# Performance work log

Measured on AMD Instinct MI355X. Metric: run time of the kernel, lower is better.

## Reference

```python
import jax, jax.numpy as jnp
import numpy as np

N_DELTA, N_THETA, N_GAMMA = 64, 128, 512
N_TOTAL = N_DELTA + N_THETA + N_GAMMA  # 704
N_CLASSES = 1000
N_STEPS = 5
DT = 0.01
COUPLING = 2.0      # coupling_strength
PAC_DT = 0.3        # delta->theta phase-amplitude coupling depth
PAC_TG = 0.3        # theta->gamma phase-amplitude coupling depth
SPARSITY = 0.1      # PhaseToRateConverter sparsity (fraction of active units)
SHARP = 10.0        # softness of the 'soft' sparsification gate
TWO_PI = 2.0 * np.pi
B = 65536


def setup_inputs() -> dict:
    key = jax.random.key(0)
    k1, k2, k3, k4 = jax.random.split(key, 4)
    x = jax.random.normal(k1, (B, N_TOTAL), dtype=jnp.float32)
    # per-sample random initial phases in [0,1), scaled to [0,2pi) inside reference
    phase0 = jax.random.uniform(k2, (B, N_TOTAL), dtype=jnp.float32)
    W = jax.random.normal(k3, (N_CLASSES, N_TOTAL), dtype=jnp.float32) * 0.02
    b = jax.random.normal(k4, (N_CLASSES,), dtype=jnp.float32) * 0.02
    return {"x": x, "phase0": phase0, "W": W, "b": b}


def _kuramoto(phi):
    # mean-field within-band Kuramoto coupling: K * mean_j sin(phi_j - phi_i)
    S = jnp.mean(jnp.sin(phi), axis=-1, keepdims=True)
    C = jnp.mean(jnp.cos(phi), axis=-1, keepdims=True)
    return COUPLING * (S * jnp.cos(phi) - C * jnp.sin(phi))


def _mean_phase(phi):
    # circular mean phase of a band, shape (B,1)
    return jnp.arctan2(jnp.mean(jnp.sin(phi), axis=-1, keepdims=True),
                       jnp.mean(jnp.cos(phi), axis=-1, keepdims=True))


def _forward(x, phase0, W, b):
    freqs = jnp.concatenate([
        jnp.linspace(1.0, 4.0, N_DELTA),    # delta band Hz
        jnp.linspace(4.0, 8.0, N_THETA),    # theta band Hz
        jnp.linspace(30.0, 80.0, N_GAMMA),  # gamma band Hz
    ]).astype(x.dtype)
    phi = phase0 * TWO_PI                       # (B, N_TOTAL)
    amp = 1.0 + jnp.abs(x) * 0.01               # amplitude seeded by |x|*0.01 on unit base
    d = slice(0, N_DELTA)
    t = slice(N_DELTA, N_DELTA + N_THETA)
    g = slice(N_DELTA + N_THETA, N_TOTAL)

    def step(carry, _):
        phi, amp = carry
        dphi = TWO_PI * freqs + jnp.concatenate(
            [_kuramoto(phi[:, d]), _kuramoto(phi[:, t]), _kuramoto(phi[:, g])], axis=-1)
        psi_d = _mean_phase(phi[:, d])
        psi_t = _mean_phase(phi[:, t])
        # PAC: theta amplitude driven by delta phase, gamma amplitude by theta phase
        damp = jnp.concatenate([
            jnp.zeros_like(amp[:, d]),
            PAC_DT * amp[:, t] * jnp.cos(psi_d),
            PAC_TG * amp[:, g] * jnp.cos(psi_t),
        ], axis=-1)
        phi_new = jnp.mod(phi + DT * dphi, TWO_PI)
        amp_new = amp + DT * damp
        return (phi_new, amp_new), None

    (phi, amp), _ = jax.lax.scan(step, (phi, amp), None, length=N_STEPS)

    # PhaseToRateConverter, mode='soft': raw rate then soft top-(sparsity) gate
    raw = amp * 0.5 * (1.0 + jnp.cos(phi))                              # (B, N_TOTAL)
    thr = jnp.quantile(raw, 1.0 - SPARSITY, axis=-1, keepdims=True)    # per-sample threshold
    rate = raw * jax.nn.sigmoid((raw - thr) * SHARP)
    return rate @ W.T + b                                               # (B, N_CLASSES)


def reference(x, phase0, W, b):
    return _forward(x, phase0, W, b)
```

## Files before the change

kernel.cpp:

```cpp
#include <hip/hip_runtime.h>

#define NB 65536
#define NTOT 704
#define NCLS 1000
#define NPAD 1024
#define KDIM 704

typedef __attribute__((ext_vector_type(8))) short bf16x8;
typedef __attribute__((ext_vector_type(4))) float f32x4;
typedef __attribute__((ext_vector_type(2))) float f32x2;

#define WB_ELEMS (NPAD * KDIM)
#define LUT_DC_OFF (2u * (WB_ELEMS + 46137344u))
#define LUT_DS_OFF (LUT_DC_OFF + NTOT * 4u)

__device__ __forceinline__ f32x2 sp(float x) { return (f32x2){x, x}; }

template <int CTRL>
__device__ __forceinline__ float dpp_shuf(float v) {
  return __int_as_float(__builtin_amdgcn_update_dpp(0, __float_as_int(v), CTRL, 0xF, 0xF, true));
}
__device__ __forceinline__ float swz16(float v) {
  return __int_as_float(__builtin_amdgcn_ds_swizzle(__float_as_int(v), 0x401F));
}
__device__ __forceinline__ float wsum_f(float v) {
  v += dpp_shuf<0xB1>(v);
  v += dpp_shuf<0x4E>(v);
  v += dpp_shuf<0x141>(v);
  v += dpp_shuf<0x140>(v);
  v += swz16(v);
  v += __shfl_xor(v, 32, 64);
  return v;
}
__device__ __forceinline__ float wmax_f(float v) {
  v = fmaxf(v, dpp_shuf<0xB1>(v));
  v = fmaxf(v, dpp_shuf<0x4E>(v));
  v = fmaxf(v, dpp_shuf<0x141>(v));
  v = fmaxf(v, dpp_shuf<0x140>(v));
  v = fmaxf(v, swz16(v));
  v = fmaxf(v, __shfl_xor(v, 32, 64));
  return v;
}
__device__ __forceinline__ float wmin_f(float v) {
  v = fminf(v, dpp_shuf<0xB1>(v));
  v = fminf(v, dpp_shuf<0x4E>(v));
  v = fminf(v, dpp_shuf<0x141>(v));
  v = fminf(v, dpp_shuf<0x140>(v));
  v = fminf(v, swz16(v));
  v = fminf(v, __shfl_xor(v, 32, 64));
  return v;
}

__device__ __forceinline__ unsigned short f2bf(float v) {
  unsigned u = __float_as_uint(v);
  u = (u + 0x7FFFu + ((u >> 16) & 1u)) >> 16;
  return (unsigned short)u;
}

__global__ __launch_bounds__(256) void convw_kernel(const float* __restrict__ W,
                                                    unsigned short* __restrict__ Wb,
                                                    float* __restrict__ dcL,
                                                    float* __restrict__ dsL) {
  int i = blockIdx.x * 256 + threadIdx.x;
  if (i < NTOT) {
    float f;
    if (i < 64)       f = 1.0f + 3.0f * (float)i * (1.0f / 63.0f);
    else if (i < 192) f = 4.0f + 4.0f * (float)(i - 64) * (1.0f / 127.0f);
    else              f = 30.0f + 50.0f * (float)(i - 192) * (1.0f / 511.0f);
    const float rev = 0.01f * f;
    dcL[i] = __builtin_amdgcn_cosf(rev);
    dsL[i] = __builtin_amdgcn_sinf(rev);
  }
  if (i >= NPAD * KDIM) return;
  int n = i / KDIM;
  float v = (n < NCLS) ? W[i] : 0.0f;
  Wb[i] = f2bf(v);
}

__global__ __launch_bounds__(256) void sim_kernel(const float* __restrict__ x,
                                                  const float* __restrict__ p0,
                                                  const float* __restrict__ dcL,
                                                  const float* __restrict__ dsL,
                                                  unsigned short* __restrict__ rateb) {
  const int wave = threadIdx.x >> 6;
  const int lane = threadIdx.x & 63;
  const int sample = blockIdx.x * 4 + wave;
  const size_t base = (size_t)sample * NTOT;

  float sD, cD, ampD, dcD, dsD;
  f32x2 sPp[5], cPp[5], dc2[5], ds2[5], amp2[5];
  {
    const float p = p0[base + lane];
    sD = __builtin_amdgcn_sinf(p);
    cD = __builtin_amdgcn_cosf(p);
    ampD = fmaf(fabsf(x[base + lane]), 0.01f, 1.0f);
    dcD = dcL[lane]; dsD = dsL[lane];
  }
#pragma unroll
  for (int pr = 0; pr < 5; ++pr) {
    const int i0 = (1 + 2 * pr) * 64 + lane;
    const int i1 = i0 + 64;
    const float pa = p0[base + i0], pb = p0[base + i1];
    sPp[pr] = (f32x2){__builtin_amdgcn_sinf(pa), __builtin_amdgcn_sinf(pb)};
    cPp[pr] = (f32x2){__builtin_amdgcn_cosf(pa), __builtin_amdgcn_cosf(pb)};
    amp2[pr] = (f32x2){fmaf(fabsf(x[base + i0]), 0.01f, 1.0f),
                       fmaf(fabsf(x[base + i1]), 0.01f, 1.0f)};
    dc2[pr] = (f32x2){dcL[i0], dcL[i1]};
    ds2[pr] = (f32x2){dsL[i0], dsL[i1]};
  }

  float prodT = 1.0f, prodG = 1.0f;

#pragma unroll
  for (int st = 0; st < 5; ++st) {
    const float Sd = wsum_f(sD);
    const float Cd = wsum_f(cD);
    const float St = wsum_f(sPp[0].x + sPp[0].y);
    const float Ct = wsum_f(cPp[0].x + cPp[0].y);
    const f32x2 gs = (sPp[1] + sPp[2]) + (sPp[3] + sPp[4]);
    const f32x2 gc = (cPp[1] + cPp[2]) + (cPp[3] + cPp[4]);
    const float Sg = wsum_f(gs.x + gs.y);
    const float Cg = wsum_f(gc.x + gc.y);
    const float cpd = Cd * __builtin_amdgcn_rsqf(fmaf(Sd, Sd, Cd * Cd));
    const float cpt = Ct * __builtin_amdgcn_rsqf(fmaf(St, St, Ct * Ct));
    prodT *= fmaf(0.003f, cpd, 1.0f);
    prodG *= fmaf(0.003f, cpt, 1.0f);
    const float sdm = Sd * (0.02f / 64.0f),  cdm = Cd * (0.02f / 64.0f);
    const float stm = St * (0.02f / 128.0f), ctm = Ct * (0.02f / 128.0f);
    const float sgm = Sg * (0.02f / 512.0f), cgm = Cg * (0.02f / 512.0f);
    {
      const float eps = fmaf(-cdm, sD, sdm * cD);
      const float cd_ = fmaf(-dsD, eps, dcD);
      const float sd_ = fmaf(dcD, eps, dsD);
      const float sn = fmaf(cD, sd_, sD * cd_);
      const float cn = fmaf(-sD, sd_, cD * cd_);
      sD = sn; cD = cn;
    }
#pragma unroll
    for (int pr = 0; pr < 5; ++pr) {
      const f32x2 Sm = sp(pr == 0 ? stm : sgm);
      const f32x2 Cm = sp(pr == 0 ? ctm : cgm);
      const f32x2 s2 = sPp[pr], c2 = cPp[pr];
      const f32x2 eps = Sm * c2 - Cm * s2;
      const f32x2 cosd = dc2[pr] - ds2[pr] * eps;
      const f32x2 sind = ds2[pr] + dc2[pr] * eps;
      sPp[pr] = s2 * cosd + c2 * sind;
      cPp[pr] = c2 * cosd - s2 * sind;
    }
  }

  float raw[11];
  unsigned kk[11];
  {
    const float h = 0.5f * ampD;
    raw[0] = fmaf(h, cD, h);
  }
  const float hT = 0.5f * prodT, hG = 0.5f * prodG;
#pragma unroll
  for (int pr = 0; pr < 5; ++pr) {
    const f32x2 h2 = amp2[pr] * sp(pr == 0 ? hT : hG);
    const f32x2 r2 = h2 * cPp[pr] + h2;
    raw[1 + 2 * pr] = r2.x;
    raw[2 + 2 * pr] = r2.y;
  }
#pragma unroll
  for (int e = 0; e < 11; ++e) kk[e] = (unsigned)(raw[e] * 8192.0f);

  unsigned pre = 0;
#pragma unroll
  for (int bit = 13; bit >= 0; --bit) {
    const unsigned u = pre | ((1u << bit) - 1u);
    int cnt = 0;
#pragma unroll
    for (int e = 0; e < 11; ++e) cnt += (int)__popcll(__ballot(kk[e] <= u));
    if (cnt < 633) pre |= (1u << bit);
  }

  int clt = 0, ceq = 0;
#pragma unroll
  for (int e = 0; e < 11; ++e) {
    clt += (int)__popcll(__ballot(kk[e] < pre));
    ceq += (int)__popcll(__ballot(kk[e] == pre));
  }

  const float qv = 0.9f * 703.0f;
  float thr;
  if (clt + ceq >= 634) {
    thr = ((float)pre + 0.5f) * (1.0f / 8192.0f);
  } else {
    float mx = -1.0f, mn = 3.0e38f;
#pragma unroll
    for (int e = 0; e < 11; ++e) {
      mx = fmaxf(mx, (kk[e] == pre) ? raw[e] : -1.0f);
      mn = fminf(mn, (kk[e] > pre) ? raw[e] : 3.0e38f);
    }
    const float S632 = wmax_f(mx);
    const float S633 = wmin_f(mn);
    thr = S632 * (633.0f - qv) + S633 * (qv - 632.0f);
  }

#pragma unroll
  for (int e = 0; e < 11; ++e) {
    const float r = raw[e];
    const float t = __expf((thr - r) * 10.0f);
    const float sg = __builtin_amdgcn_rcpf(1.0f + t);
    rateb[base + e * 64 + lane] = f2bf(r * sg);
  }
}

#define BM2 256
#define BN2 256
#define BK2 32
#define NK2 (KDIM / BK2)

__device__ __forceinline__ void gload16(const unsigned short* g, unsigned short* l) {
  __builtin_amdgcn_global_load_lds((const __attribute__((address_space(1))) void*)g,
                                   (__attribute__((address_space(3))) void*)l,
                                   16, 0, 0);
}

__global__ __launch_bounds__(512) void gemm_kernel(const unsigned short* __restrict__ A,
                                                   const unsigned short* __restrict__ Bw,
                                                   const float* __restrict__ bias,
                                                   float* __restrict__ C) {
  __shared__ __align__(16) unsigned short lsA[3 * BM2 * BK2];
  __shared__ __align__(16) unsigned short lsB[3 * BN2 * BK2];
  const int tid  = threadIdx.x;
  const int wave = tid >> 6;
  const int lane = tid & 63;

  const int bid = blockIdx.x;
  const int swz = (bid & 7) * 128 + (bid >> 3);
  const int bm = swz >> 2;
  const int bn = swz & 3;

  const int wr = wave >> 2;
  const int wc = wave & 3;

  f32x4 acc[8][4];
#pragma unroll
  for (int i = 0; i < 8; ++i)
#pragma unroll
    for (int j = 0; j < 4; ++j) acc[i][j] = (f32x4){0.f, 0.f, 0.f, 0.f};

  const int rowi = tid >> 2;
  const int ksrc = (tid & 3) ^ ((tid >> 3) & 3);

  const unsigned short* Abase = A  + (size_t)(bm * BM2) * KDIM;
  const unsigned short* Bbase = Bw + (size_t)(bn * BN2) * KDIM;

#define STAGE2(buf, kt)                                                        \
  {                                                                            \
    const int k0_ = (kt) * BK2;                                                \
    _Pragma("unroll")                                                          \
    for (int g_ = 0; g_ < 2; ++g_) {                                           \
      gload16(Abase + (size_t)(g_ * 128 + rowi) * KDIM + k0_ + ksrc * 8,       \
              lsA + (buf) * (BM2 * BK2) + g_ * 4096 + tid * 8);                \
      gload16(Bbase + (size_t)(g_ * 128 + rowi) * KDIM + k0_ + ksrc * 8,       \
              lsB + (buf) * (BN2 * BK2) + g_ * 4096 + tid * 8);                \
    }                                                                          \
  }

  STAGE2(0, 0);
  STAGE2(1, 1);

  const int l15 = lane & 15;
  const int kq  = lane >> 4;

  int cur = 0;
#pragma unroll 1
  for (int t = 0; t < NK2; ++t) {
    int sb = cur + 2; if (sb >= 3) sb -= 3;
    if (t < NK2 - 2) STAGE2(sb, t + 2);
    if (t < NK2 - 2)      asm volatile("s_waitcnt vmcnt(8)" ::: "memory");
    else if (t == NK2 - 2) asm volatile("s_waitcnt vmcnt(4)" ::: "memory");
    else                   asm volatile("s_waitcnt vmcnt(0)" ::: "memory");
    asm volatile("s_barrier" ::: "memory");

    bf16x8 af[8], bf[4];
    const unsigned short* la = lsA + cur * (BM2 * BK2);
    const unsigned short* lb = lsB + cur * (BN2 * BK2);
#pragma unroll
    for (int m = 0; m < 8; ++m) {
      const int row = wr * 128 + m * 16 + l15;
      const int slot = kq ^ ((row >> 1) & 3);
      af[m] = *(const bf16x8*)&la[row * BK2 + slot * 8];
    }
#pragma unroll
    for (int n = 0; n < 4; ++n) {
      const int row = wc * 64 + n * 16 + l15;
      const int slot = kq ^ ((row >> 1) & 3);
      bf[n] = *(const bf16x8*)&lb[row * BK2 + slot * 8];
    }
    asm volatile("s_waitcnt lgkmcnt(0)" ::: "memory");
    __builtin_amdgcn_s_setprio(1);
#pragma unroll
    for (int m = 0; m < 8; ++m)
#pragma unroll
      for (int n = 0; n < 4; ++n)
        acc[m][n] = __builtin_amdgcn_mfma_f32_16x16x32_bf16(af[m], bf[n], acc[m][n], 0, 0, 0);
    __builtin_amdgcn_s_setprio(0);
    asm volatile("s_barrier" ::: "memory");
    cur += 1; if (cur >= 3) cur -= 3;
  }

  const int crow0 = bm * BM2 + wr * 128;
  const int ccol0 = bn * BN2 + wc * 64;
  const int rql = (lane >> 4) * 4;
  const int cl  = lane & 15;
#pragma unroll
  for (int n = 0; n < 4; ++n) {
    const int col = ccol0 + n * 16 + cl;
    if (col < NCLS) {
      const float bb = bias[col];
#pragma unroll
      for (int m = 0; m < 8; ++m) {
#pragma unroll
        for (int r = 0; r < 4; ++r) {
          const int row = crow0 + m * 16 + rql + r;
          C[(size_t)row * NCLS + col] = acc[m][n][r] + bb;
        }
      }
    }
  }
}

extern "C" void kernel_launch(void* const* d_in, const int* in_sizes, int n_in,
                              void* d_out, int out_size, void* d_ws, size_t ws_size,
                              hipStream_t stream) {
  const float* x    = (const float*)d_in[0];
  const float* p0   = (const float*)d_in[1];
  const float* W    = (const float*)d_in[2];
  const float* bias = (const float*)d_in[3];
  float* out = (float*)d_out;

  unsigned short* Wb    = (unsigned short*)d_ws;
  unsigned short* rateb = (unsigned short*)d_ws + WB_ELEMS;
  float* dcL = (float*)((char*)d_ws + LUT_DC_OFF);
  float* dsL = (float*)((char*)d_ws + LUT_DS_OFF);

  convw_kernel<<<dim3((NPAD * KDIM + 255) / 256), dim3(256), 0, stream>>>(W, Wb, dcL, dsL);
  sim_kernel<<<dim3(NB / 4), dim3(256), 0, stream>>>(x, p0, dcL, dsL, rateb);
  gemm_kernel<<<dim3((NB / BM2) * (NPAD / BN2)), dim3(512), 0, stream>>>(rateb, Wb, bias, out);
}
```

Baseline: 331.3 us.

## Restructure bf16 GEMM mainloop into BK=64 double-buffered four-phase interleaved schedule

The GEMM main loop moves from a BK=32 triple-buffered pipeline to BK=64 with double buffering. Each k-step is split into four MFMA quarter-tiles, with one global-to-LDS half-tile load for the next step issued between them, so loads and compute interleave inside the iteration. The LDS swizzle changes to an 8-way XOR to match the 64-wide rows, and the launch bounds now request 2 blocks per CU. The costs are more barriers per iteration, 128KB of LDS per block (which likely defeats the 2-block occupancy hint), and a tighter register budget that could cause spills.

```diff
diff --git a/kernel.cpp b/kernel.cpp
--- a/kernel.cpp
+++ b/kernel.cpp
@@ -208,10 +208,8 @@
   }
 }
 
-#define BM2 256
-#define BN2 256
-#define BK2 32
-#define NK2 (KDIM / BK2)
+#define BK3 64
+#define NK3 (KDIM / BK3)
 
 __device__ __forceinline__ void gload16(const unsigned short* g, unsigned short* l) {
   __builtin_amdgcn_global_load_lds((const __attribute__((address_space(1))) void*)g,
@@ -219,12 +217,12 @@
                                    16, 0, 0);
 }
 
-__global__ __launch_bounds__(512) void gemm_kernel(const unsigned short* __restrict__ A,
-                                                   const unsigned short* __restrict__ Bw,
-                                                   const float* __restrict__ bias,
-                                                   float* __restrict__ C) {
-  __shared__ __align__(16) unsigned short lsA[3 * BM2 * BK2];
-  __shared__ __align__(16) unsigned short lsB[3 * BN2 * BK2];
+__global__ __launch_bounds__(512, 2) void gemm_kernel(const unsigned short* __restrict__ A,
+                                                      const unsigned short* __restrict__ Bw,
+                                                      const float* __restrict__ bias,
+                                                      float* __restrict__ C) {
+  __shared__ __align__(16) unsigned short lsA[4 * 8192];
+  __shared__ __align__(16) unsigned short lsB[4 * 8192];
   const int tid  = threadIdx.x;
   const int wave = tid >> 6;
   const int lane = tid & 63;
@@ -243,69 +241,121 @@
 #pragma unroll
     for (int j = 0; j < 4; ++j) acc[i][j] = (f32x4){0.f, 0.f, 0.f, 0.f};
 
-  const int rowi = tid >> 2;
-  const int ksrc = (tid & 3) ^ ((tid >> 3) & 3);
-
-  const unsigned short* Abase = A  + (size_t)(bm * BM2) * KDIM;
-  const unsigned short* Bbase = Bw + (size_t)(bn * BN2) * KDIM;
-
-#define STAGE2(buf, kt)                                                        \
-  {                                                                            \
-    const int k0_ = (kt) * BK2;                                                \
-    _Pragma("unroll")                                                          \
-    for (int g_ = 0; g_ < 2; ++g_) {                                           \
-      gload16(Abase + (size_t)(g_ * 128 + rowi) * KDIM + k0_ + ksrc * 8,       \
-              lsA + (buf) * (BM2 * BK2) + g_ * 4096 + tid * 8);                \
-      gload16(Bbase + (size_t)(g_ * 128 + rowi) * KDIM + k0_ + ksrc * 8,       \
-              lsB + (buf) * (BN2 * BK2) + g_ * 4096 + tid * 8);                \
-    }                                                                          \
-  }
-
-  STAGE2(0, 0);
-  STAGE2(1, 1);
+  const int srow = tid >> 3;
+  const int sc16 = ((tid & 7) ^ (srow & 7)) * 8;
+  const unsigned short* Ab = A  + (size_t)(bm * 256) * KDIM;
+  const unsigned short* Bb = Bw + (size_t)(bn * 256) * KDIM;
+
+#define SHALF(dst, srcb, rb, k0)                                                      \
+  gload16((srcb) + (size_t)((rb) + srow) * KDIM + (k0) + sc16, (dst) + tid * 8);      \
+  gload16((srcb) + (size_t)((rb) + 64 + srow) * KDIM + (k0) + sc16, (dst) + 4096 + tid * 8);
+
+  SHALF(lsA + 0 * 8192, Ab, 0, 0)
+  SHALF(lsA + 1 * 8192, Ab, 128, 0)
+  SHALF(lsB + 0 * 8192, Bb, 0, 0)
+  SHALF(lsB + 1 * 8192, Bb, 128, 0)
 
   const int l15 = lane & 15;
   const int kq  = lane >> 4;
 
-  int cur = 0;
+  bf16x8 af[4][2];
+  bf16x8 bg[4][2];
+
 #pragma unroll 1
-  for (int t = 0; t < NK2; ++t) {
-    int sb = cur + 2; if (sb >= 3) sb -= 3;
-    if (t < NK2 - 2) STAGE2(sb, t + 2);
-    if (t < NK2 - 2)      asm volatile("s_waitcnt vmcnt(8)" ::: "memory");
-    else if (t == NK2 - 2) asm volatile("s_waitcnt vmcnt(4)" ::: "memory");
-    else                   asm volatile("s_waitcnt vmcnt(0)" ::: "memory");
-    asm volatile("s_barrier" ::: "memory");
-
-    bf16x8 af[8], bf[4];
-    const unsigned short* la = lsA + cur * (BM2 * BK2);
-    const unsigned short* lb = lsB + cur * (BN2 * BK2);
-#pragma unroll
-    for (int m = 0; m < 8; ++m) {
-      const int row = wr * 128 + m * 16 + l15;
-      const int slot = kq ^ ((row >> 1) & 3);
-      af[m] = *(const bf16x8*)&la[row * BK2 + slot * 8];
-    }
-#pragma unroll
-    for (int n = 0; n < 4; ++n) {
-      const int row = wc * 64 + n * 16 + l15;
-      const int slot = kq ^ ((row >> 1) & 3);
-      bf[n] = *(const bf16x8*)&lb[row * BK2 + slot * 8];
+  for (int t = 0; t < NK3; ++t) {
+    const int d = t & 1, nd = d ^ 1;
+    const int k0n = (t + 1) * BK3;
+    const unsigned short* hA = lsA + (d * 2 + wr) * 8192;
+    const unsigned short* hB = lsB + (d * 2 + (wc >> 1)) * 8192;
+    const int rB0 = (wc & 1) * 64;
+
+    if (t < NK3 - 1) {
+      SHALF(lsA + (nd * 2 + 0) * 8192, Ab, 0, k0n)
+      asm volatile("s_waitcnt vmcnt(2)" ::: "memory");
+    } else {
+      asm volatile("s_waitcnt vmcnt(0)" ::: "memory");
+    }
+    asm volatile("s_barrier" ::: "memory");
+#pragma unroll
+    for (int m = 0; m < 4; ++m) {
+      const int lr = m * 16 + l15;
+      af[m][0] = *(const bf16x8*)&hA[lr * 64 + ((kq ^ (lr & 7)) * 8)];
+      af[m][1] = *(const bf16x8*)&hA[lr * 64 + (((kq + 4) ^ (lr & 7)) * 8)];
+    }
+#pragma unroll
+    for (int n = 0; n < 2; ++n) {
+      const int lr = rB0 + n * 16 + l15;
+      bg[n][0] = *(const bf16x8*)&hB[lr * 64 + ((kq ^ (lr & 7)) * 8)];
+      bg[n][1] = *(const bf16x8*)&hB[lr * 64 + (((kq + 4) ^ (lr & 7)) * 8)];
     }
     asm volatile("s_waitcnt lgkmcnt(0)" ::: "memory");
     __builtin_amdgcn_s_setprio(1);
 #pragma unroll
-    for (int m = 0; m < 8; ++m)
-#pragma unroll
-      for (int n = 0; n < 4; ++n)
-        acc[m][n] = __builtin_amdgcn_mfma_f32_16x16x32_bf16(af[m], bf[n], acc[m][n], 0, 0, 0);
+    for (int m = 0; m < 4; ++m)
+#pragma unroll
+      for (int n = 0; n < 2; ++n) {
+        acc[m][n] = __builtin_amdgcn_mfma_f32_16x16x32_bf16(af[m][0], bg[n][0], acc[m][n], 0, 0, 0);
+        acc[m][n] = __builtin_amdgcn_mfma_f32_16x16x32_bf16(af[m][1], bg[n][1], acc[m][n], 0, 0, 0);
+      }
     __builtin_amdgcn_s_setprio(0);
     asm volatile("s_barrier" ::: "memory");
-    cur += 1; if (cur >= 3) cur -= 3;
-  }
-
-  const int crow0 = bm * BM2 + wr * 128;
-  const int ccol0 = bn * BN2 + wc * 64;
+
+#pragma unroll
+    for (int n = 2; n < 4; ++n) {
+      const int lr = rB0 + n * 16 + l15;
+      bg[n][0] = *(const bf16x8*)&hB[lr * 64 + ((kq ^ (lr & 7)) * 8)];
+      bg[n][1] = *(const bf16x8*)&hB[lr * 64 + (((kq + 4) ^ (lr & 7)) * 8)];
+    }
+    if (t < NK3 - 1) { SHALF(lsA + (nd * 2 + 1) * 8192, Ab, 128, k0n) }
+    asm volatile("s_barrier" ::: "memory");
+    asm volatile("s_waitcnt lgkmcnt(0)" ::: "memory");
+    __builtin_amdgcn_s_setprio(1);
+#pragma unroll
+    for (int m = 0; m < 4; ++m)
+#pragma unroll
+      for (int n = 2; n < 4; ++n) {
+        acc[m][n] = __builtin_amdgcn_mfma_f32_16x16x32_bf16(af[m][0], bg[n][0], acc[m][n], 0, 0, 0);
+        acc[m][n] = __builtin_amdgcn_mfma_f32_16x16x32_bf16(af[m][1], bg[n][1], acc[m][n], 0, 0, 0);
+      }
+    __builtin_amdgcn_s_setprio(0);
+    asm volatile("s_barrier" ::: "memory");
+
+#pragma unroll
+    for (int m = 0; m < 4; ++m) {
+      const int lr = (m + 4) * 16 + l15;
+      af[m][0] = *(const bf16x8*)&hA[lr * 64 + ((kq ^ (lr & 7)) * 8)];
+      af[m][1] = *(const bf16x8*)&hA[lr * 64 + (((kq + 4) ^ (lr & 7)) * 8)];
+    }
+    if (t < NK3 - 1) { SHALF(lsB + (nd * 2 + 0) * 8192, Bb, 0, k0n) }
+    asm volatile("s_barrier" ::: "memory");
+    asm volatile("s_waitcnt lgkmcnt(0)" ::: "memory");
+    __builtin_amdgcn_s_setprio(1);
+#pragma unroll
+    for (int m = 0; m < 4; ++m)
+#pragma unroll
+      for (int n = 0; n < 2; ++n) {
+        acc[m + 4][n] = __builtin_amdgcn_mfma_f32_16x16x32_bf16(af[m][0], bg[n][0], acc[m + 4][n], 0, 0, 0);
+        acc[m + 4][n] = __builtin_amdgcn_mfma_f32_16x16x32_bf16(af[m][1], bg[n][1], acc[m + 4][n], 0, 0, 0);
+      }
+    __builtin_amdgcn_s_setprio(0);
+    asm volatile("s_barrier" ::: "memory");
+
+    if (t < NK3 - 1) { SHALF(lsB + (nd * 2 + 1) * 8192, Bb, 128, k0n) }
+    asm volatile("s_barrier" ::: "memory");
+    __builtin_amdgcn_s_setprio(1);
+#pragma unroll
+    for (int m = 0; m < 4; ++m)
+#pragma unroll
+      for (int n = 2; n < 4; ++n) {
+        acc[m + 4][n] = __builtin_amdgcn_mfma_f32_16x16x32_bf16(af[m][0], bg[n][0], acc[m + 4][n], 0, 0, 0);
+        acc[m + 4][n] = __builtin_amdgcn_mfma_f32_16x16x32_bf16(af[m][1], bg[n][1], acc[m + 4][n], 0, 0, 0);
+      }
+    __builtin_amdgcn_s_setprio(0);
+    asm volatile("s_barrier" ::: "memory");
+  }
+
+  const int crow0 = bm * 256 + wr * 128;
+  const int ccol0 = bn * 256 + wc * 64;
   const int rql = (lane >> 4) * 4;
   const int cl  = lane & 15;
 #pragma unroll
@@ -341,5 +391,5 @@
 
   convw_kernel<<<dim3((NPAD * KDIM + 255) / 256), dim3(256), 0, stream>>>(W, Wb, dcL, dsL);
   sim_kernel<<<dim3(NB / 4), dim3(256), 0, stream>>>(x, p0, dcL, dsL, rateb);
-  gemm_kernel<<<dim3((NB / BM2) * (NPAD / BN2)), dim3(512), 0, stream>>>(rateb, Wb, bias, out);
-}
+  gemm_kernel<<<dim3((NB / 256) * (NPAD / 256)), dim3(512), 0, stream>>>(rateb, Wb, bias, out);
+}
```

Result: faster. 324.0 us (-2.2%).
